# Optimization experiments

Hardware: AMD Instinct MI355X
Metric: run time of the kernel (lower is better)

## Reference

```python
import jax, jax.numpy as jnp
import numpy as np
from jax import lax

TAU = 0.05
N_ITERS = 4
TOPL = 64


def l2norm(x, axis):
    return x / (jnp.linalg.norm(x, axis=axis, keepdims=True) + 1e-6)


def setup_inputs() -> dict:
    key = jax.random.key(0)
    ks = jax.random.split(key, 8)
    B, N, Ck, Cv, H, W, L = 2, 4, 64, 512, 64, 64, 256
    qk = jax.random.normal(ks[0], (B, Ck, H, W), jnp.float32)
    qv = jax.random.normal(ks[1], (B, Cv, H, W), jnp.float32)
    qv_mem = jax.random.normal(ks[2], (B, N, Cv, H, W), jnp.float32)
    masks = jax.random.uniform(ks[3], (B, N, 2, H, W), jnp.float32)
    # random_init: normal(0, sqrt(2/L)) then l2norm over Ck (dim=-2)
    kappa0 = jax.random.normal(ks[4], (B, N, 2, Ck, L), jnp.float32) * np.sqrt(2.0 / L).astype(np.float32)
    kappa0 = l2norm(kappa0, axis=-2)
    nu0 = jnp.zeros((B, N, 2, Cv, L), jnp.float32)
    zita0 = jnp.full((B, N, 2, 1, L), 1e-6, jnp.float32)
    Cin = 2 * Cv + 2 * TOPL  # 1152
    Wf = jax.random.normal(ks[5], (Cv, Cin, 3, 3), jnp.float32) * 0.02
    bf = jnp.zeros((Cv,), jnp.float32)
    Wa = jax.random.normal(ks[6], (Cv, Cin, 3, 3), jnp.float32) * 0.02
    ba = jnp.zeros((Cv,), jnp.float32)
    return {"qk": qk, "qv": qv, "qv_mem": qv_mem, "masks": masks,
            "kappa0": kappa0, "nu0": nu0, "zita0": zita0,
            "Wf": Wf, "bf": bf, "Wa": Wa, "ba": ba}


def reference(qk, qv, qv_mem, masks, kappa0, nu0, zita0, Wf, bf, Wa, ba):
    B, Ck, H, W = qk.shape
    N = masks.shape[1]
    Cv = qv.shape[1]
    L = kappa0.shape[-1]
    HW = H * W

    # ---- swem: EM iterations (torch runs these under no_grad) ----
    x = qk.reshape(B, 1, 1, Ck, HW)            # (B,1,1,Ck,HW)
    m = masks.reshape(B, N, 2, HW, 1)          # (B,N,2,HW,1)
    x_t = jnp.swapaxes(x, -2, -1)              # (B,1,1,HW,Ck)
    x_t_n = l2norm(x_t, axis=-1)

    weights = m
    kappa = kappa0
    z = None
    zita = None
    for i in range(N_ITERS):
        # swe_step: softmax((z - max)/tau) == softmax(z/tau), stable
        kn = l2norm(kappa, axis=-2)
        zz = jnp.matmul(x_t, kn)               # (B,N,2,HW,L)
        zz = jax.nn.softmax(zz / TAU, axis=-1) * weights
        # swm_step
        zita = zita0 + zz.sum(axis=-2, keepdims=True)            # (B,N,2,1,L)
        kappa = (zita0 * kappa0 + jnp.matmul(x, zz)) / zita      # (B,N,2,Ck,L)
        z = zz
        if i < N_ITERS - 1:
            # sww_step
            kn = l2norm(kappa, axis=-2)
            s = jnp.matmul(x_t_n, kn)                            # (B,N,2,HW,L)
            mx = jnp.max(s, axis=-1, keepdims=True)
            mx = jnp.max(mx, axis=2, keepdims=True)
            s_exp = jnp.exp((s - mx) / TAU)
            sum_exp = s_exp.sum(axis=-1, keepdims=True)          # (B,N,2,HW,1)
            props = sum_exp / sum_exp.sum(axis=2, keepdims=True)
            weights = m * (1.0 - props)

    mv_flat = qv_mem.reshape(B, N, 1, Cv, HW)                    # (B,N,1,Cv,HW)
    nu = (zita0 * nu0 + jnp.matmul(mv_flat, z)) / zita           # (B,N,2,Cv,L)

    # ---- matching / get_affinity ----
    qk_n = l2norm(qk, axis=1)
    mk = l2norm(kappa, axis=-2)
    qk_ = qk_n.reshape(B, 1, 1, Ck, HW)
    aff = jnp.matmul(jnp.swapaxes(mk, -2, -1), qk_)              # (B,N,2,L,HW)
    mx = jnp.max(aff, axis=2, keepdims=True)
    mx = jnp.max(mx, axis=3, keepdims=True)
    exp_aff = jnp.exp((aff - mx) / TAU)
    p_aff = exp_aff / exp_aff.sum(axis=(2, 3), keepdims=True)
    p_aff = p_aff.reshape(B, N, 2 * L, HW)

    # ---- perm_inv_feat: top-l over L, cumulative sums (vectorized) ----
    ea = exp_aff.reshape(B * N, 2, L, H, W)
    sorted_aff = lax.top_k(jnp.moveaxis(ea, 2, -1), TOPL)[0]     # (BN,2,H,W,TOPL) desc
    feat = jnp.cumsum(sorted_aff, axis=-1)
    Sf = feat[:, 0] / (feat[:, 0] + feat[:, 1])                  # (BN,H,W,TOPL)
    Sf = jnp.moveaxis(Sf, -1, 1)                                 # (BN,TOPL,H,W)
    S = jnp.concatenate([Sf, 1.0 - Sf], axis=1)                  # (BN,2*TOPL,H,W)

    # ---- memory readout ----
    mv2 = jnp.swapaxes(nu, 2, 3).reshape(B, N, Cv, 2 * L)
    mem_out = jnp.matmul(mv2, p_aff).reshape(B * N, Cv, H, W)

    qv_e = jnp.broadcast_to(qv[:, None], (B, N, Cv, H, W)).reshape(B * N, Cv, H, W)
    fin = jnp.concatenate([mem_out, qv_e, S], axis=1)            # (BN, 2*Cv+2*TOPL, H, W)

    # ---- FeatureFusionLayer: gated 3x3 convs ----
    dn = ('NCHW', 'OIHW', 'NCHW')
    f = lax.conv_general_dilated(fin, Wf, (1, 1), 'SAME', dimension_numbers=dn) + bf[None, :, None, None]
    a = lax.conv_general_dilated(fin, Wa, (1, 1), 'SAME', dimension_numbers=dn) + ba[None, :, None, None]
    return f * jax.nn.sigmoid(a)
```

## Files before the change

### kernel.cpp

```cpp
#include <hip/hip_runtime.h>
#include <hip/hip_bf16.h>
#include <math.h>


typedef __attribute__((ext_vector_type(8))) short bf16x8;
typedef __attribute__((ext_vector_type(4))) float f32x4;
typedef __attribute__((ext_vector_type(16))) float f32x16;

static __device__ __forceinline__ short f2b(float f){
  __hip_bfloat16 h = __float2bfloat16(f);
  short s; __builtin_memcpy(&s, &h, 2); return s;
}
static __device__ __forceinline__ unsigned pack2(float lo, float hi){
  return (unsigned)(unsigned short)f2b(lo) | ((unsigned)(unsigned short)f2b(hi) << 16);
}

static __device__ __forceinline__ float wred_max(float v){
  #pragma unroll
  for (int off = 32; off > 0; off >>= 1) v = fmaxf(v, __shfl_xor(v, off));
  return v;
}
static __device__ __forceinline__ float wred_sum(float v){
  #pragma unroll
  for (int off = 32; off > 0; off >>= 1) v += __shfl_xor(v, off);
  return v;
}

static __device__ __forceinline__ void gload_lds16(const short* g, short* l){
  __builtin_amdgcn_global_load_lds((const __attribute__((address_space(1))) unsigned int*)(g),
                                   (__attribute__((address_space(3))) unsigned int*)(l),
                                   16, 0, 0);
}

#define FMA16(X0,X1,X2,X3,KV) \
  acc[0]+=X0.x*KV; acc[1]+=X0.y*KV; acc[2]+=X0.z*KV; acc[3]+=X0.w*KV; \
  acc[4]+=X1.x*KV; acc[5]+=X1.y*KV; acc[6]+=X1.z*KV; acc[7]+=X1.w*KV; \
  acc[8]+=X2.x*KV; acc[9]+=X2.y*KV; acc[10]+=X2.z*KV; acc[11]+=X2.w*KV; \
  acc[12]+=X3.x*KV; acc[13]+=X3.y*KV; acc[14]+=X3.z*KV; acc[15]+=X3.w*KV;


__global__ void k_prep_x(const float* __restrict__ qk, float* __restrict__ xT, float* __restrict__ xTn){
  int idx = blockIdx.x*256 + threadIdx.x;
  int b = idx >> 12, hw = idx & 4095;
  float v[64]; float ss = 0.f;
  #pragma unroll
  for (int k=0;k<64;k++){ v[k] = qk[((size_t)b*64 + k)*4096 + hw]; ss += v[k]*v[k]; }
  float inv = 1.f/(sqrtf(ss) + 1e-6f);
  #pragma unroll
  for (int k=0;k<64;k++){ xT[(size_t)idx*64 + k] = v[k]; xTn[(size_t)idx*64 + k] = v[k]*inv; }
}

__global__ void k_init_w_kn(const float* __restrict__ masks, const float* __restrict__ kappa0,
                            float* __restrict__ wts, float* __restrict__ kn){
  int t = blockIdx.x*256 + threadIdx.x;
  if (t < 16*4096) wts[t] = masks[t];
  if (t < 16*256){
    int bng = t >> 8, l = t & 255;
    float ss = 0.f;
    #pragma unroll 4
    for (int k=0;k<64;k++){ float v = kappa0[((size_t)bng*64 + k)*256 + l]; ss += v*v; }
    float inv = 1.f/(sqrtf(ss) + 1e-6f);
    #pragma unroll 4
    for (int k=0;k<64;k++) kn[((size_t)bng*64 + k)*256 + l] = kappa0[((size_t)bng*64 + k)*256 + l]*inv;
  }
}

__global__ void k_prep_wt2(const float* __restrict__ Wsrc, short* __restrict__ Wt2, int conv){
  int t = blockIdx.x*256 + threadIdx.x;
  int j = t & 7;
  int cvl = (t >> 3) & 63;
  int kh = (t >> 9) & 1;
  int rest = t >> 10;
  int r = rest % 9;
  int tile = rest / 9;
  int cb = tile % 72;
  int cvb = tile / 72;
  int cv = cvb*64 + cvl;
  int cin = cb*16 + kh*8 + j;
  Wt2[((size_t)tile*2 + conv)*9216 + (r*2 + kh)*512 + cvl*8 + j] = f2b(Wsrc[((size_t)cv*1152 + cin)*9 + r]);
}

__global__ void k_qv_fin(const float* __restrict__ qv, unsigned* __restrict__ fin32){
  int t = blockIdx.x*256 + threadIdx.x;
  int bn = t >> 20;
  int rem = t & 1048575;
  int p = rem >> 12;
  int hw = rem & 4095;
  int b = bn >> 2;
  float lo = qv[((size_t)b*512 + 2*p)*4096 + hw];
  float hi = qv[((size_t)b*512 + 2*p + 1)*4096 + hw];
  fin32[(size_t)bn*2359296 + (size_t)(256 + p)*4096 + hw] = pack2(lo, hi);
}


__global__ __launch_bounds__(256) void k_zz(const float* __restrict__ xT, const float* __restrict__ kn,
                                            const float* __restrict__ wts, float* __restrict__ zzb){
  int blk = blockIdx.x;
  int bng = blk >> 8;
  int hw0 = (blk & 255) * 16;
  int b = bng >> 3;
  int t = threadIdx.x;
  int lane = t & 63, wid = t >> 6;
  __shared__ float xs[64][16];
  __shared__ float redm[4], reds[4];
  {
    int k = t & 63, pq = t >> 6;
    #pragma unroll
    for (int p = pq; p < 16; p += 4)
      xs[k][p] = xT[((size_t)b*4096 + hw0 + p)*64 + k];
  }
  float acc[16];
  #pragma unroll
  for (int p=0;p<16;p++) acc[p] = 0.f;
  __syncthreads();
  const float* knp = kn + (size_t)bng*16384 + t;
  #pragma unroll 2
  for (int k=0;k<64;k++){
    float knv = knp[k*256];
    float4 x0 = *(const float4*)&xs[k][0];
    float4 x1 = *(const float4*)&xs[k][4];
    float4 x2 = *(const float4*)&xs[k][8];
    float4 x3 = *(const float4*)&xs[k][12];
    FMA16(x0,x1,x2,x3,knv)
  }
  #pragma unroll
  for (int p=0;p<16;p++){
    float v = acc[p];
    float m = wred_max(v);
    if (lane==0) redm[wid] = m;
    __syncthreads();
    m = fmaxf(fmaxf(redm[0],redm[1]), fmaxf(redm[2],redm[3]));
    float e = __expf((v - m) * 20.0f);
    float s = wred_sum(e);
    if (lane==0) reds[wid] = s;
    __syncthreads();
    s = reds[0]+reds[1]+reds[2]+reds[3];
    float wgt = wts[bng*4096 + hw0 + p];
    zzb[((size_t)bng*4096 + hw0 + p)*256 + t] = e/s*wgt;
  }
}

__global__ __launch_bounds__(1024) void k_part(const float* __restrict__ qk, const float* __restrict__ zzb,
                                               float* __restrict__ kpart, float* __restrict__ zpart){
  int bng = blockIdx.x >> 4, ch = blockIdx.x & 15;
  int b = bng >> 3;
  int t = threadIdx.x; int l = t & 255; int kq = t >> 8;
  __shared__ float xs[64][80];
  float acc[16];
  #pragma unroll
  for (int j=0;j<16;j++) acc[j]=0.f;
  float zs = 0.f;
  for (int sc=0; sc<4; sc++){
    int hwb = ch*256 + sc*64;
    __syncthreads();
    {
      int hw_l = t & 63, kk = t >> 6;
      #pragma unroll
      for (int k = kk; k < 64; k += 16)
        xs[hw_l][k] = qk[((size_t)b*64 + k)*4096 + hwb + hw_l];
    }
    __syncthreads();
    #pragma unroll 2
    for (int hw_l=0; hw_l<64; hw_l++){
      float zv = zzb[((size_t)bng*4096 + hwb + hw_l)*256 + l];
      zs += zv;
      const float* xp = &xs[hw_l][kq*16];
      float4 x0 = *(const float4*)(xp);
      float4 x1 = *(const float4*)(xp+4);
      float4 x2 = *(const float4*)(xp+8);
      float4 x3 = *(const float4*)(xp+12);
      FMA16(x0,x1,x2,x3,zv)
    }
  }
  #pragma unroll
  for (int j=0;j<16;j++)
    kpart[(((size_t)bng*16 + ch)*64 + kq*16 + j)*256 + l] = acc[j];
  if (kq == 0) zpart[((size_t)bng*16 + ch)*256 + l] = zs;
}

__global__ __launch_bounds__(1024) void k_fin(const float* __restrict__ kpart, const float* __restrict__ zpart,
                                              const float* __restrict__ kappa0, const float* __restrict__ zita0,
                                              float* __restrict__ kn, float* __restrict__ zita){
  int bng = blockIdx.x; int t = threadIdx.x; int l = t & 255; int kq = t >> 8;
  float z0 = zita0[bng*256 + l];
  float zs = z0;
  #pragma unroll
  for (int ch=0; ch<16; ch++) zs += zpart[((size_t)bng*16 + ch)*256 + l];
  if (kq==0) zita[bng*256 + l] = zs;
  float inv = 1.f/zs;
  float kap[16]; float ss = 0.f;
  #pragma unroll
  for (int j=0;j<16;j++){
    int k = kq*16 + j;
    float a = z0 * kappa0[((size_t)bng*64 + k)*256 + l];
    #pragma unroll
    for (int ch=0; ch<16; ch++) a += kpart[(((size_t)bng*16 + ch)*64 + k)*256 + l];
    float kv = a*inv; kap[j] = kv; ss += kv*kv;
  }
  __shared__ float ssr[4][256];
  ssr[kq][l] = ss;
  __syncthreads();
  float tot = ssr[0][l]+ssr[1][l]+ssr[2][l]+ssr[3][l];
  float ninv = 1.f/(sqrtf(tot) + 1e-6f);
  #pragma unroll
  for (int j=0;j<16;j++) kn[((size_t)bng*64 + kq*16 + j)*256 + l] = kap[j]*ninv;
}

__global__ __launch_bounds__(512) void k_sww(const float* __restrict__ xTn, const float* __restrict__ kn,
                                             const float* __restrict__ masks, float* __restrict__ wts){
  int blk = blockIdx.x;
  int bnI = blk >> 8;
  int hw0 = (blk & 255)*16;
  int b = bnI >> 2;
  int t = threadIdx.x;
  int lane = t & 63, wid = t >> 6;
  int g = t >> 8; int l = t & 255;
  int bng = bnI*2 + g;
  __shared__ float xs[64][16];
  __shared__ float redm[8], reds[8];
  {
    int k = t & 63, pq = t >> 6;
    #pragma unroll
    for (int p = pq; p < 16; p += 8)
      xs[k][p] = xTn[((size_t)b*4096 + hw0 + p)*64 + k];
  }
  float knr[64];
  const float* knp = kn + (size_t)bng*16384 + l;
  #pragma unroll
  for (int k=0;k<64;k++) knr[k] = knp[k*256];
  float acc[16];
  #pragma unroll
  for (int p=0;p<16;p++) acc[p]=0.f;
  __syncthreads();
  #pragma unroll 2
  for (int k=0;k<64;k++){
    float knv = knr[k];
    float4 x0 = *(const float4*)&xs[k][0];
    float4 x1 = *(const float4*)&xs[k][4];
    float4 x2 = *(const float4*)&xs[k][8];
    float4 x3 = *(const float4*)&xs[k][12];
    FMA16(x0,x1,x2,x3,knv)
  }
  #pragma unroll
  for (int p=0;p<16;p++){
    float v = acc[p];
    float m = wred_max(v);
    if (lane==0) redm[wid] = m;
    __syncthreads();
    m = fmaxf(fmaxf(fmaxf(redm[0],redm[1]),fmaxf(redm[2],redm[3])),
              fmaxf(fmaxf(redm[4],redm[5]),fmaxf(redm[6],redm[7])));
    float e = __expf((v - m) * 20.0f);
    float s = wred_sum(e);
    if (lane==0) reds[wid] = s;
    __syncthreads();
    float s0 = reds[0]+reds[1]+reds[2]+reds[3];
    float s1 = reds[4]+reds[5]+reds[6]+reds[7];
    if (lane==0 && (wid==0 || wid==4)){
      float sg = g ? s1 : s0;
      wts[bng*4096 + hw0 + p] = masks[bng*4096 + hw0 + p]*(1.f - sg/(s0+s1));
    }
  }
}

__global__ __launch_bounds__(512) void k_aff(const float* __restrict__ xTn, const float* __restrict__ kn,
                                             float* __restrict__ paff){
  int blk = blockIdx.x;
  int bnI = blk >> 8;
  int hw0 = (blk & 255)*16;
  int b = bnI >> 2;
  int t = threadIdx.x;
  int lane = t & 63, wid = t >> 6;
  int g = t >> 8; int l = t & 255;
  int bng = bnI*2 + g;
  __shared__ float xs[64][16];
  __shared__ float redm[8], reds[8];
  {
    int k = t & 63, pq = t >> 6;
    #pragma unroll
    for (int p = pq; p < 16; p += 8)
      xs[k][p] = xTn[((size_t)b*4096 + hw0 + p)*64 + k];
  }
  float knr[64];
  const float* knp = kn + (size_t)bng*16384 + l;
  #pragma unroll
  for (int k=0;k<64;k++) knr[k] = knp[k*256];
  float acc[16];
  #pragma unroll
  for (int p=0;p<16;p++) acc[p]=0.f;
  __syncthreads();
  #pragma unroll 2
  for (int k=0;k<64;k++){
    float knv = knr[k];
    float4 x0 = *(const float4*)&xs[k][0];
    float4 x1 = *(const float4*)&xs[k][4];
    float4 x2 = *(const float4*)&xs[k][8];
    float4 x3 = *(const float4*)&xs[k][12];
    FMA16(x0,x1,x2,x3,knv)
  }
  #pragma unroll
  for (int p=0;p<16;p++){
    float v = acc[p];
    float m = wred_max(v);
    if (lane==0) redm[wid] = m;
    __syncthreads();
    m = fmaxf(fmaxf(fmaxf(redm[0],redm[1]),fmaxf(redm[2],redm[3])),
              fmaxf(fmaxf(redm[4],redm[5]),fmaxf(redm[6],redm[7])));
    float e = __expf((v - m) * 20.0f);
    float s = wred_sum(e);
    if (lane==0) reds[wid] = s;
    __syncthreads();
    float tot = reds[0]+reds[1]+reds[2]+reds[3]+reds[4]+reds[5]+reds[6]+reds[7];
    paff[((size_t)bnI*4096 + hw0 + p)*512 + t] = e/tot;
  }
}


static __device__ __forceinline__ float topk_cum(float va, float vb, float vc, float vd, int lane){
  float run = 0.f, cme = 0.f;
  #pragma unroll 2
  for (int tt=0; tt<64; tt++){
    float m = fmaxf(fmaxf(va,vb), fmaxf(vc,vd));
    float wm = wred_max(m);
    run += wm;
    if (lane == tt) cme = run;
    unsigned long long ball = __ballot(m == wm);
    int wl = __ffsll(ball) - 1;
    if (lane == wl){
      if (va == wm) va = -1.f;
      else if (vb == wm) vb = -1.f;
      else if (vc == wm) vc = -1.f;
      else vd = -1.f;
    }
  }
  return cme;
}

__global__ __launch_bounds__(256) void k_topk(const float* __restrict__ paff, unsigned* __restrict__ fin32){
  int wid = threadIdx.x >> 6, lane = threadIdx.x & 63;
  int px = blockIdx.x*4 + wid;
  int bn = px >> 12, hw = px & 4095;
  const float* row = paff + (size_t)px*512;
  float4 a0 = *(const float4*)(row + lane*4);
  float4 a1 = *(const float4*)(row + 256 + lane*4);
  float c0 = topk_cum(a0.x,a0.y,a0.z,a0.w, lane);
  float c1 = topk_cum(a1.x,a1.y,a1.z,a1.w, lane);
  float sf = c0/(c0+c1);
  float sf2 = __shfl_down(sf, 1);
  if (!(lane & 1)){
    size_t base = (size_t)bn*2359296;
    fin32[base + (size_t)(512 + (lane>>1))*4096 + hw] = pack2(sf, sf2);
    fin32[base + (size_t)(544 + (lane>>1))*4096 + hw] = pack2(1.f - sf, 1.f - sf2);
  }
}


__global__ __launch_bounds__(256) void k_nu(const float* __restrict__ qvm, const float* __restrict__ zzb,
                                            const float* __restrict__ nu0, const float* __restrict__ zita0,
                                            const float* __restrict__ zita, short* __restrict__ mv2){
  constexpr int AP = 40;
  __shared__ short lA[64*AP];
  __shared__ short lB[64*AP];
  int blk = blockIdx.x;
  int bng = blk >> 5, cvb = (blk >> 2) & 7, lb = blk & 3;
  int bn = bng >> 1, g = bng & 1;
  int t = threadIdx.x, lane = t & 63, w = t >> 6;
  int wm = w >> 1, wn = w & 1;
  int quad = lane >> 4, fr = lane & 15;
  f32x4 acc[2][2] = {};
  const float* Ab = qvm + ((size_t)bn*512 + cvb*64)*4096;
  const float* Bb = zzb + (size_t)bng*4096*256 + lb*64;
  int arow = t >> 2, acg = (t & 3)*8;
  int bhw = t & 31, blg = (t >> 5)*8;
  for (int k0 = 0; k0 < 4096; k0 += 32){
    __syncthreads();
    {
      const float* s = Ab + (size_t)arow*4096 + k0 + acg;
      float4 f0 = *(const float4*)s, f1 = *(const float4*)(s+4);
      bf16x8 v;
      v[0]=f2b(f0.x); v[1]=f2b(f0.y); v[2]=f2b(f0.z); v[3]=f2b(f0.w);
      v[4]=f2b(f1.x); v[5]=f2b(f1.y); v[6]=f2b(f1.z); v[7]=f2b(f1.w);
      *(bf16x8*)&lA[arow*AP + acg] = v;
    }
    {
      const float* s = Bb + (size_t)(k0 + bhw)*256 + blg;
      float4 f0 = *(const float4*)s, f1 = *(const float4*)(s+4);
      lB[(blg+0)*AP + bhw] = f2b(f0.x);
      lB[(blg+1)*AP + bhw] = f2b(f0.y);
      lB[(blg+2)*AP + bhw] = f2b(f0.z);
      lB[(blg+3)*AP + bhw] = f2b(f0.w);
      lB[(blg+4)*AP + bhw] = f2b(f1.x);
      lB[(blg+5)*AP + bhw] = f2b(f1.y);
      lB[(blg+6)*AP + bhw] = f2b(f1.z);
      lB[(blg+7)*AP + bhw] = f2b(f1.w);
    }
    __syncthreads();
    int koff = quad*8;
    bf16x8 a0 = *(const bf16x8*)&lA[(wm*32 +  0 + fr)*AP + koff];
    bf16x8 a1 = *(const bf16x8*)&lA[(wm*32 + 16 + fr)*AP + koff];
    bf16x8 b0 = *(const bf16x8*)&lB[(wn*32 +  0 + fr)*AP + koff];
    bf16x8 b1 = *(const bf16x8*)&lB[(wn*32 + 16 + fr)*AP + koff];
    acc[0][0] = __builtin_amdgcn_mfma_f32_16x16x32_bf16(a0,b0,acc[0][0],0,0,0);
    acc[0][1] = __builtin_amdgcn_mfma_f32_16x16x32_bf16(a0,b1,acc[0][1],0,0,0);
    acc[1][0] = __builtin_amdgcn_mfma_f32_16x16x32_bf16(a1,b0,acc[1][0],0,0,0);
    acc[1][1] = __builtin_amdgcn_mfma_f32_16x16x32_bf16(a1,b1,acc[1][1],0,0,0);
  }
  #pragma unroll
  for (int mf=0; mf<2; mf++)
  #pragma unroll
  for (int nf=0; nf<2; nf++)
  #pragma unroll
  for (int r=0;r<4;r++){
    int cv = cvb*64 + wm*32 + mf*16 + quad*4 + r;
    int l  = lb*64 + wn*32 + nf*16 + fr;
    float c = acc[mf][nf][r];
    float z0 = zita0[bng*256 + l];
    float nv = (z0 * nu0[((size_t)bng*512 + cv)*256 + l] + c) / zita[bng*256 + l];
    mv2[((size_t)bn*512 + cv)*512 + g*256 + l] = f2b(nv);
  }
}

__global__ __launch_bounds__(256) void k_mem(const short* __restrict__ mv2, const float* __restrict__ paff,
                                             unsigned* __restrict__ fin32){
  constexpr int BP = 40;
  __shared__ short lB[256*BP];
  int blk = blockIdx.x;
  int bn = blk >> 7, cvb = (blk >> 4) & 7, hwb = blk & 15;
  int t = threadIdx.x, lane = t & 63, w = t >> 6;
  int quad = lane >> 4, fr = lane & 15;
  f32x4 acc[4][4] = {};
  const short* Ab = mv2 + ((size_t)bn*512 + cvb*64)*512;
  const float* Bb = paff + ((size_t)bn*4096 + hwb*256)*512;
  for (int k0=0; k0<512; k0+=32){
    __syncthreads();
    {
      const float* s = Bb + (size_t)t*512 + k0;
      #pragma unroll
      for (int q=0;q<4;q++){
        float4 f0 = *(const float4*)(s + q*8);
        float4 f1 = *(const float4*)(s + q*8 + 4);
        bf16x8 v;
        v[0]=f2b(f0.x); v[1]=f2b(f0.y); v[2]=f2b(f0.z); v[3]=f2b(f0.w);
        v[4]=f2b(f1.x); v[5]=f2b(f1.y); v[6]=f2b(f1.z); v[7]=f2b(f1.w);
        *(bf16x8*)&lB[t*BP + q*8] = v;
      }
    }
    __syncthreads();
    int koff = quad*8;
    bf16x8 af[4];
    #pragma unroll
    for (int mf=0; mf<4; mf++)
      af[mf] = *(const bf16x8*)(Ab + (size_t)(mf*16 + fr)*512 + k0 + koff);
    #pragma unroll
    for (int nf=0; nf<4; nf++){
      bf16x8 bv = *(const bf16x8*)&lB[(w*64 + nf*16 + fr)*BP + koff];
      #pragma unroll
      for (int mf=0; mf<4; mf++)
        acc[mf][nf] = __builtin_amdgcn_mfma_f32_16x16x32_bf16(af[mf], bv, acc[mf][nf],0,0,0);
    }
  }
  #pragma unroll
  for (int mf=0;mf<4;mf++)
  #pragma unroll
  for (int nf=0;nf<4;nf++){
    int hw = hwb*256 + w*64 + nf*16 + fr;
    int p0 = cvb*32 + mf*8 + quad*2;
    unsigned lo = pack2(acc[mf][nf][0], acc[mf][nf][1]);
    unsigned hi = pack2(acc[mf][nf][2], acc[mf][nf][3]);
    fin32[(size_t)bn*2359296 + (size_t)p0*4096 + hw] = lo;
    fin32[(size_t)bn*2359296 + (size_t)(p0+1)*4096 + hw] = hi;
  }
}

__global__ __launch_bounds__(256, 2) void k_conv(const unsigned* __restrict__ fin32,
                                                 const short* __restrict__ Wt2,
                                                 const float* __restrict__ bfv, const float* __restrict__ bav,
                                                 float* __restrict__ out){
  __shared__ __attribute__((aligned(16))) unsigned lFu[2*6*66*4];
  __shared__ __attribute__((aligned(16))) short wbuf[2*9216];
  int blk = blockIdx.x;
  int bn = blk >> 7, cvb = (blk >> 4) & 7, yb = blk & 15;
  int t = threadIdx.x, lane = t & 63, wv = t >> 6;
  int ln = lane & 31, kh = lane >> 5;
  int y0 = yb*4;
  f32x16 accF[2][2] = {}, accA[2][2] = {};
  const unsigned* finB = fin32 + (size_t)bn*2359296;
  const short* Wslice = Wt2 + (size_t)cvb*72*18432;
  if (t < 96){
    int pj = t & 3; int side = (t >> 2) & 1; int row = (t >> 3) % 6; int khz = t / 48;
    lFu[((khz*6 + row)*66 + (side ? 65 : 0))*4 + pj] = 0u;
  }
  int sx = lane;
  for (int cb = 0; cb < 72; cb++){
    unsigned stg[3][4];
    #pragma unroll
    for (int i = 0; i < 3; i++){
      int tk = wv*3 + i;
      int skh = (tk >= 6) ? 1 : 0;
      int srow = tk - skh*6;
      int gy = y0 - 1 + srow;
      bool ok = (gy >= 0 && gy < 64);
      #pragma unroll
      for (int pj = 0; pj < 4; pj++)
        stg[i][pj] = ok ? finB[(size_t)(cb*8 + skh*4 + pj)*4096 + gy*64 + sx] : 0u;
    }
    __syncthreads();
    #pragma unroll
    for (int i = 0; i < 3; i++){
      int tk = wv*3 + i;
      int skh = (tk >= 6) ? 1 : 0;
      int srow = tk - skh*6;
      uint4 v; v.x = stg[i][0]; v.y = stg[i][1]; v.z = stg[i][2]; v.w = stg[i][3];
      *(uint4*)&lFu[((skh*6 + srow)*66 + sx + 1)*4] = v;
    }
    {
      const short* src = Wslice + (size_t)cb*18432 + lane*8;
      #pragma unroll
      for (int i = 0; i < 9; i++){
        int idx = wv*9 + i;
        gload_lds16(src + idx*512, &wbuf[idx*512]);
      }
    }
    __syncthreads();
    const short* wfb = wbuf;
    const short* wab = wbuf + 9216;
    #pragma unroll 3
    for (int r9 = 0; r9 < 9; r9++){
      int dy = r9/3, dx = r9 - dy*3;
      bf16x8 f0 = *(const bf16x8*)(wfb + r9*1024 + kh*512 + ln*8);
      bf16x8 f1 = *(const bf16x8*)(wfb + r9*1024 + kh*512 + ln*8 + 256);
      bf16x8 a0 = *(const bf16x8*)(wab + r9*1024 + kh*512 + ln*8);
      bf16x8 a1 = *(const bf16x8*)(wab + r9*1024 + kh*512 + ln*8 + 256);
      int row = wv + dy;
      #pragma unroll
      for (int xh = 0; xh < 2; xh++){
        bf16x8 bv = *(const bf16x8*)((const short*)lFu + (((kh*6 + row)*66 + xh*32 + ln + dx)*8));
        accF[0][xh] = __builtin_amdgcn_mfma_f32_32x32x16_bf16(f0, bv, accF[0][xh],0,0,0);
        accF[1][xh] = __builtin_amdgcn_mfma_f32_32x32x16_bf16(f1, bv, accF[1][xh],0,0,0);
        accA[0][xh] = __builtin_amdgcn_mfma_f32_32x32x16_bf16(a0, bv, accA[0][xh],0,0,0);
        accA[1][xh] = __builtin_amdgcn_mfma_f32_32x32x16_bf16(a1, bv, accA[1][xh],0,0,0);
      }
    }
  }
  int y = y0 + wv;
  #pragma unroll
  for (int mf = 0; mf < 2; mf++)
  #pragma unroll
  for (int xh = 0; xh < 2; xh++){
    int x = xh*32 + ln;
    #pragma unroll
    for (int reg = 0; reg < 16; reg++){
      int cv = cvb*64 + mf*32 + 4*kh + 8*(reg>>2) + (reg&3);
      float fv = accF[mf][xh][reg] + bfv[cv];
      float av = accA[mf][xh][reg] + bav[cv];
      out[((size_t)bn*512 + cv)*4096 + (size_t)y*64 + x] = fv/(1.f + __expf(-av));
    }
  }
}


extern "C" void kernel_launch(void* const* d_in, const int* in_sizes, int n_in,
                              void* d_out, int out_size, void* d_ws, size_t ws_size,
                              hipStream_t stream){
  const float* qk     = (const float*)d_in[0];
  const float* qv     = (const float*)d_in[1];
  const float* qvm    = (const float*)d_in[2];
  const float* masks  = (const float*)d_in[3];
  const float* kappa0 = (const float*)d_in[4];
  const float* nu0    = (const float*)d_in[5];
  const float* zita0  = (const float*)d_in[6];
  const float* Wf     = (const float*)d_in[7];
  const float* bfb    = (const float*)d_in[8];
  const float* Wa     = (const float*)d_in[9];
  const float* bab    = (const float*)d_in[10];
  float* out = (float*)d_out;

  float* ws    = (float*)d_ws;
  float* zzb   = ws;
  float* kpart = zzb + 16777216;
  float* zpart = kpart + 4194304;
  float* kn    = zpart + 65536;
  float* zita  = kn + 262144;
  float* wts   = zita + 4096;
  float* xT    = wts + 65536;
  float* xTn   = xT + 524288;
  short* mv2   = (short*)(xTn + 524288);
  unsigned* fin32 = (unsigned*)(mv2 + 4194304);
  short* Wt2   = (short*)(fin32 + 18874368);

  k_prep_x<<<32, 256, 0, stream>>>(qk, xT, xTn);
  k_init_w_kn<<<256, 256, 0, stream>>>(masks, kappa0, wts, kn);
  k_prep_wt2<<<20736, 256, 0, stream>>>(Wf, Wt2, 0);
  k_prep_wt2<<<20736, 256, 0, stream>>>(Wa, Wt2, 1);
  k_qv_fin<<<32768, 256, 0, stream>>>(qv, fin32);

  for (int it = 0; it < 4; ++it){
    k_zz<<<4096, 256, 0, stream>>>(xT, kn, wts, zzb);
    k_part<<<256, 1024, 0, stream>>>(qk, zzb, kpart, zpart);
    k_fin<<<16, 1024, 0, stream>>>(kpart, zpart, kappa0, zita0, kn, zita);
    if (it < 3) k_sww<<<2048, 512, 0, stream>>>(xTn, kn, masks, wts);
  }

  k_nu<<<512, 256, 0, stream>>>(qvm, zzb, nu0, zita0, zita, mv2);
  k_aff<<<2048, 512, 0, stream>>>(xTn, kn, zzb );
  k_topk<<<8192, 256, 0, stream>>>(zzb, fin32);
  k_mem<<<1024, 256, 0, stream>>>(mv2, zzb, fin32);
  k_conv<<<1024, 256, 0, stream>>>(fin32, Wt2, bfb, bab, out);
}
```

Baseline: 2.366 ms.

## Software-pipeline conv kernel with double-buffered activations and split weight DMA

Restructures the k_conv main loop so the activation tile lives in a double-buffered LDS array and the per-channel-block weight DMA is split into two halves. The second half of the current block's weights and the first half of the next block's weights are fetched while MFMAs run on the already-resident half. The next activation tile's global loads are issued before the second compute phase and written to the alternate buffer afterwards. This aims to hide global-memory and DMA latency behind MFMA work. The cost is extra LDS and more live staging registers, plus correctness that relies on barriers draining the async LDS loads.

```diff
diff --git a/kernel.cpp b/kernel.cpp
--- a/kernel.cpp
+++ b/kernel.cpp
@@ -475,7 +475,7 @@
                                                  const short* __restrict__ Wt2,
                                                  const float* __restrict__ bfv, const float* __restrict__ bav,
                                                  float* __restrict__ out){
-  __shared__ __attribute__((aligned(16))) unsigned lFu[2*6*66*4];
+  __shared__ __attribute__((aligned(16))) unsigned lFu[2][2*6*66*4];
   __shared__ __attribute__((aligned(16))) short wbuf[2*9216];
   int blk = blockIdx.x;
   int bn = blk >> 7, cvb = (blk >> 4) & 7, yb = blk & 15;
@@ -485,62 +485,90 @@
   f32x16 accF[2][2] = {}, accA[2][2] = {};
   const unsigned* finB = fin32 + (size_t)bn*2359296;
   const short* Wslice = Wt2 + (size_t)cvb*72*18432;
-  if (t < 96){
-    int pj = t & 3; int side = (t >> 2) & 1; int row = (t >> 3) % 6; int khz = t / 48;
-    lFu[((khz*6 + row)*66 + (side ? 65 : 0))*4 + pj] = 0u;
-  }
-  int sx = lane;
+  if (t < 192){
+    int pj = t & 3; int side = (t >> 2) & 1; int row = (t >> 3) % 6; int khz = (t / 48) & 1; int buf = t / 96;
+    lFu[buf][((khz*6 + row)*66 + (side ? 65 : 0))*4 + pj] = 0u;
+  }
+  int tks[3], tkh[3], tgy[3];
+  #pragma unroll
+  for (int i = 0; i < 3; i++){
+    int tk = wv*3 + i;
+    tkh[i] = (tk >= 6) ? 1 : 0;
+    tks[i] = tk - tkh[i]*6;
+    tgy[i] = y0 - 1 + tks[i];
+  }
+  unsigned stg[3][4];
+
+#define LOAD_STG(CB) { \
+    _Pragma("unroll") \
+    for (int i = 0; i < 3; i++){ \
+      bool ok = (tgy[i] >= 0 && tgy[i] < 64); \
+      _Pragma("unroll") \
+      for (int pj = 0; pj < 4; pj++) \
+        stg[i][pj] = ok ? finB[(size_t)((CB)*8 + tkh[i]*4 + pj)*4096 + tgy[i]*64 + lane] : 0u; \
+    } }
+#define WRITE_STG(BUF) { \
+    _Pragma("unroll") \
+    for (int i = 0; i < 3; i++){ \
+      uint4 v; v.x = stg[i][0]; v.y = stg[i][1]; v.z = stg[i][2]; v.w = stg[i][3]; \
+      *(uint4*)&lFu[BUF][((tkh[i]*6 + tks[i])*66 + lane + 1)*4] = v; \
+    } }
+#define DMA_H0(CB) { \
+    const short* src = Wslice + (size_t)(CB)*18432 + lane*8; \
+    _Pragma("unroll") \
+    for (int j = 0; j < 5; j++){ \
+      int i = wv*5 + j; \
+      int idx = (i < 10) ? i : i + 8; \
+      gload_lds16(src + idx*512, &wbuf[idx*512]); \
+    } }
+#define DMA_H1(CB) { \
+    const short* src = Wslice + (size_t)(CB)*18432 + lane*8; \
+    _Pragma("unroll") \
+    for (int j = 0; j < 4; j++){ \
+      int i = wv*4 + j; \
+      int idx = (i < 8) ? i + 10 : i + 20; \
+      gload_lds16(src + idx*512, &wbuf[idx*512]); \
+    } }
+#define CONV_COMPUTE(R9LO, R9HI, BUF) { \
+    _Pragma("unroll") \
+    for (int r9 = (R9LO); r9 < (R9HI); r9++){ \
+      int dy = r9/3, dx = r9 - dy*3; \
+      bf16x8 f0 = *(const bf16x8*)(wbuf + r9*1024 + kh*512 + ln*8); \
+      bf16x8 f1 = *(const bf16x8*)(wbuf + r9*1024 + kh*512 + ln*8 + 256); \
+      bf16x8 a0 = *(const bf16x8*)(wbuf + 9216 + r9*1024 + kh*512 + ln*8); \
+      bf16x8 a1 = *(const bf16x8*)(wbuf + 9216 + r9*1024 + kh*512 + ln*8 + 256); \
+      int row = wv + dy; \
+      _Pragma("unroll") \
+      for (int xh = 0; xh < 2; xh++){ \
+        bf16x8 bv = *(const bf16x8*)((const short*)&lFu[BUF][0] + (((kh*6 + row)*66 + xh*32 + ln + dx)*8)); \
+        accF[0][xh] = __builtin_amdgcn_mfma_f32_32x32x16_bf16(f0, bv, accF[0][xh],0,0,0); \
+        accF[1][xh] = __builtin_amdgcn_mfma_f32_32x32x16_bf16(f1, bv, accF[1][xh],0,0,0); \
+        accA[0][xh] = __builtin_amdgcn_mfma_f32_32x32x16_bf16(a0, bv, accA[0][xh],0,0,0); \
+        accA[1][xh] = __builtin_amdgcn_mfma_f32_32x32x16_bf16(a1, bv, accA[1][xh],0,0,0); \
+      } \
+    } }
+
+  LOAD_STG(0)
+  WRITE_STG(0)
+  DMA_H0(0)
+  int cur = 0;
   for (int cb = 0; cb < 72; cb++){
-    unsigned stg[3][4];
-    #pragma unroll
-    for (int i = 0; i < 3; i++){
-      int tk = wv*3 + i;
-      int skh = (tk >= 6) ? 1 : 0;
-      int srow = tk - skh*6;
-      int gy = y0 - 1 + srow;
-      bool ok = (gy >= 0 && gy < 64);
-      #pragma unroll
-      for (int pj = 0; pj < 4; pj++)
-        stg[i][pj] = ok ? finB[(size_t)(cb*8 + skh*4 + pj)*4096 + gy*64 + sx] : 0u;
-    }
-    __syncthreads();
-    #pragma unroll
-    for (int i = 0; i < 3; i++){
-      int tk = wv*3 + i;
-      int skh = (tk >= 6) ? 1 : 0;
-      int srow = tk - skh*6;
-      uint4 v; v.x = stg[i][0]; v.y = stg[i][1]; v.z = stg[i][2]; v.w = stg[i][3];
-      *(uint4*)&lFu[((skh*6 + srow)*66 + sx + 1)*4] = v;
-    }
-    {
-      const short* src = Wslice + (size_t)cb*18432 + lane*8;
-      #pragma unroll
-      for (int i = 0; i < 9; i++){
-        int idx = wv*9 + i;
-        gload_lds16(src + idx*512, &wbuf[idx*512]);
-      }
-    }
-    __syncthreads();
-    const short* wfb = wbuf;
-    const short* wab = wbuf + 9216;
-    #pragma unroll 3
-    for (int r9 = 0; r9 < 9; r9++){
-      int dy = r9/3, dx = r9 - dy*3;
-      bf16x8 f0 = *(const bf16x8*)(wfb + r9*1024 + kh*512 + ln*8);
-      bf16x8 f1 = *(const bf16x8*)(wfb + r9*1024 + kh*512 + ln*8 + 256);
-      bf16x8 a0 = *(const bf16x8*)(wab + r9*1024 + kh*512 + ln*8);
-      bf16x8 a1 = *(const bf16x8*)(wab + r9*1024 + kh*512 + ln*8 + 256);
-      int row = wv + dy;
-      #pragma unroll
-      for (int xh = 0; xh < 2; xh++){
-        bf16x8 bv = *(const bf16x8*)((const short*)lFu + (((kh*6 + row)*66 + xh*32 + ln + dx)*8));
-        accF[0][xh] = __builtin_amdgcn_mfma_f32_32x32x16_bf16(f0, bv, accF[0][xh],0,0,0);
-        accF[1][xh] = __builtin_amdgcn_mfma_f32_32x32x16_bf16(f1, bv, accF[1][xh],0,0,0);
-        accA[0][xh] = __builtin_amdgcn_mfma_f32_32x32x16_bf16(a0, bv, accA[0][xh],0,0,0);
-        accA[1][xh] = __builtin_amdgcn_mfma_f32_32x32x16_bf16(a1, bv, accA[1][xh],0,0,0);
-      }
-    }
-  }
+    __syncthreads();
+    DMA_H1(cb)
+    CONV_COMPUTE(0, 5, cur)
+    __syncthreads();
+    int nx = (cb < 71) ? cb + 1 : 71;
+    LOAD_STG(nx)
+    if (cb < 71) DMA_H0(cb + 1)
+    CONV_COMPUTE(5, 9, cur)
+    WRITE_STG(cur ^ 1)
+    cur ^= 1;
+  }
+#undef LOAD_STG
+#undef WRITE_STG
+#undef DMA_H0
+#undef DMA_H1
+#undef CONV_COMPUTE
   int y = y0 + wv;
   #pragma unroll
   for (int mf = 0; mf < 2; mf++)
```

Result: no change. 2.367 ms (+0.0%).
